# Optimization experiments

Measured on AMD Instinct MI355X. Metric: run time of the kernel, lower is better.

Reference implementation:

```python
import jax, jax.numpy as jnp
import numpy as np

EPS = 1e-12  # tf.nn.l2_normalize epsilon used inside keras CosineSimilarity


def _cos(a, b):
    # keras CosineSimilarity returns -cos; callers negate explicitly.
    an = a / jnp.sqrt(jnp.maximum(jnp.sum(a * a, axis=-1, keepdims=True), EPS))
    bn = b / jnp.sqrt(jnp.maximum(jnp.sum(b * b, axis=-1, keepdims=True), EPS))
    return jnp.sum(an * bn, axis=-1)


def setup_inputs() -> dict:
    key = jax.random.key(0)
    B, S, D, H, N = 1024, 200, 128, 128, 64
    ks = jax.random.split(key, 8)
    X_series = jax.random.normal(ks[0], (B, S, D), jnp.float32)
    pos_series = jax.random.normal(ks[1], (S, D), jnp.float32)
    X_item = jax.random.normal(ks[2], (B, D), jnp.float32)
    origin = jax.random.normal(ks[3], (B, N, D), jnp.float32)  # X_negative
    # contiguous-prefix validity mask (module assumes valid positions form a prefix)
    lengths = jax.random.randint(ks[4], (B,), 1, S + 1)
    valid_mask = jnp.arange(S)[None, :] < lengths[:, None]
    # learned params (GlorotUniform-scale init)
    Wp = jax.random.normal(ks[5], (D, H), jnp.float32) * 0.08
    We = jax.random.normal(ks[6], (D, H), jnp.float32) * 0.08
    z = jax.random.normal(ks[7], (H,), jnp.float32) * 0.1
    return {"X_series": X_series, "pos_series": pos_series, "X_item": X_item,
            "valid_mask": valid_mask, "origin": origin, "Wp": Wp, "We": We, "z": z}


def reference(X_series, pos_series, X_item, valid_mask, origin, Wp, We, z):
    B, S, D = X_series.shape
    # additive tanh attention: z . tanh(X_series @ We + pos_series @ Wp)
    hidden = jnp.tanh(jnp.einsum('bsd,dh->bsh', X_series, We) + (pos_series @ Wp)[None])
    scores = jnp.einsum('bsh,h->bs', hidden, z)
    scores = jnp.where(valid_mask, scores, -jnp.inf)
    attn = jax.nn.softmax(scores, axis=-1)                      # [B,S]
    attentioned = attn[:, :, None] * X_series                    # [B,S,D]
    attention_output = jnp.sum(attentioned, axis=1)              # [B,D]
    inner = jnp.sum(attention_output * X_item, axis=-1, keepdims=True)
    concated = jnp.concatenate([attention_output, inner], axis=1)  # [B,D+1]

    # ---- auxiliary loss ----
    last_idx = jnp.sum(valid_mask.astype(jnp.int32), axis=1) - 1
    last_vec = attentioned[jnp.arange(B), last_idx]              # gather_nd
    new_mask = (jnp.arange(S)[None, :] < last_idx[:, None]).astype(X_series.dtype)
    out_vec = jnp.sum(attentioned * new_mask[:, :, None], axis=1)  # [B,D]
    # keras CosineSimilarity = -cos_sim; then mapped to (x+1)/2 and used as logits
    pos_logits = (-_cos(last_vec, out_vec) + 1.0) / 2.0          # [B]
    neg_logits = (-_cos(origin, out_vec[:, None, :]) + 1.0) / 2.0  # [B,N]
    pos_loss = jax.nn.softplus(-pos_logits)  # sigmoid_xent labels=1
    neg_loss = jax.nn.softplus(neg_logits)   # sigmoid_xent labels=0
    # NB: TF reduces pos_loss over its only axis -> scalar, broadcast-added to [B]
    auxiliary_loss = jnp.sum(pos_loss) + jnp.sum(neg_loss, axis=-1)  # [B]
    return concated, auxiliary_loss
```

## Files before the change

kernel.cpp:

```cpp
#include <hip/hip_runtime.h>
#include <hip/hip_bf16.h>
#include <math.h>

#define B_ 1024
#define S_ 200
#define D_ 128
#define H_ 128
#define N_ 64

typedef __attribute__((ext_vector_type(8))) short short8;
typedef __attribute__((ext_vector_type(8))) __bf16 bf16x8;
typedef __attribute__((ext_vector_type(4))) float floatx4;

static __device__ __forceinline__ float bf2f(unsigned short u) {
    union { unsigned int i; float f; } v; v.i = ((unsigned int)u) << 16; return v.f;
}
static __device__ __forceinline__ unsigned short f2bf(float f) {
    union { float f; unsigned int u; } v; v.f = f;
    unsigned int u = v.u;
    return (unsigned short)((u + 0x7FFFu + ((u >> 16) & 1u)) >> 16);
}
static __device__ __forceinline__ float ld1(const void* p, int isbf, size_t i) {
    return isbf ? bf2f(((const unsigned short*)p)[i]) : ((const float*)p)[i];
}
static __device__ __forceinline__ float fast_tanh(float x) {
    float t = __expf(2.0f * x);
    return 1.0f - 2.0f * __builtin_amdgcn_rcpf(t + 1.0f);
}

__global__ __launch_bounds__(64) void detect_kernel(
    const void* a0, const void* a1, const void* a2, const void* a3,
    const void* a4, const void* a5, const void* a6, const void* a7,
    int* flags)
{
    int bid = blockIdx.x, t = threadIdx.x;
    if (bid == 3) {
        const unsigned char* mb = (const unsigned char*)a3;
        int f = 0;
        for (int i = t; i < 4096; i += 64)
            if ((i & 3) && mb[i]) f = 1;
        for (int off = 32; off; off >>= 1) f |= __shfl_xor(f, off, 64);
        if (t == 0) flags[3] = f;
        return;
    }
    const void* ptrs[8] = {a0, a1, a2, a3, a4, a5, a6, a7};
    const int counts[8] = {B_*S_*D_, S_*D_, B_*D_, 0, B_*N_*D_, D_*H_, D_*H_, H_};
    const unsigned int* w = (const unsigned int*)ptrs[bid];
    int words = counts[bid] / 2; if (words > 1024) words = 1024;
    int pass = 0, tot = 0;
    for (int i = t; i < words; i += 64) {
        unsigned int e = (w[i] >> 7) & 0xFF;
        tot++;
        if (e == 0 || (e >= 96 && e <= 140)) pass++;
    }
    for (int off = 32; off; off >>= 1) {
        pass += __shfl_xor(pass, off, 64);
        tot  += __shfl_xor(tot,  off, 64);
    }
    if (t == 0) flags[bid] = (pass * 4 >= tot * 3) ? 1 : 0;
}

__global__ __launch_bounds__(1024) void prep_kernel(
    const void* __restrict__ We, const int* __restrict__ flags,
    unsigned short* __restrict__ WeT)
{
    __shared__ unsigned short T[128][136];
    int t = threadIdx.x;
    int fWe = flags[6];
    for (int c = t; c < 2048; c += 1024) {
        int d = c >> 4, h8 = (c & 15) * 8;
        short8 v;
        if (fWe) {
            v = *(const short8*)((const unsigned short*)We + d * H_ + h8);
        } else {
            const float* p = (const float*)We + d * H_ + h8;
            float4 a = ((const float4*)p)[0], b = ((const float4*)p)[1];
            v[0] = (short)f2bf(a.x); v[1] = (short)f2bf(a.y);
            v[2] = (short)f2bf(a.z); v[3] = (short)f2bf(a.w);
            v[4] = (short)f2bf(b.x); v[5] = (short)f2bf(b.y);
            v[6] = (short)f2bf(b.z); v[7] = (short)f2bf(b.w);
        }
        *(short8*)(&T[d][h8]) = v;
    }
    __syncthreads();
    for (int c = t; c < 2048; c += 1024) {
        int h = c >> 4, d8 = (c & 15) * 8;
        short8 v;
#pragma unroll
        for (int j = 0; j < 8; ++j) v[j] = (short)T[d8 + j][h];
        *(short8*)(WeT + h * D_ + d8) = v;
    }
}

__global__ __launch_bounds__(128) void pb_kernel(
    const void* __restrict__ pos, const void* __restrict__ Wp,
    const int* __restrict__ flags, float* __restrict__ pb)
{
    int s = blockIdx.x, h = threadIdx.x;
    int fpos = flags[1], fWp = flags[5];
    __shared__ float prow[D_];
    prow[h] = ld1(pos, fpos, (size_t)s * D_ + h);
    __syncthreads();
    float acc = 0.f;
    if (fWp) {
        const unsigned short* W = (const unsigned short*)Wp;
        for (int d = 0; d < D_; ++d) acc = fmaf(prow[d], bf2f(W[d * H_ + h]), acc);
    } else {
        const float* W = (const float*)Wp;
        for (int d = 0; d < D_; ++d) acc = fmaf(prow[d], W[d * H_ + h], acc);
    }
    pb[s * H_ + h] = acc;
}

__global__ __launch_bounds__(256) void scores_kernel(
    const void* __restrict__ Xs, const unsigned short* __restrict__ WeT,
    const void* __restrict__ zv, const float* __restrict__ pb,
    const int* __restrict__ flags, float* __restrict__ scores)
{
    int t = threadIdx.x;
    int lane = t & 63, w = t >> 6;
    int quad = lane >> 4, mrow = lane & 15;
    int fXs = flags[0], fz = flags[7];
    int row0 = blockIdx.x * 128 + w * 32;

    float zl[8];
#pragma unroll
    for (int nt = 0; nt < 8; ++nt) zl[nt] = ld1(zv, fz, nt * 16 + mrow);

    floatx4 acc[2][8];
#pragma unroll
    for (int mt = 0; mt < 2; ++mt)
#pragma unroll
        for (int nt = 0; nt < 8; ++nt) {
            acc[mt][nt][0] = 0.f; acc[mt][nt][1] = 0.f;
            acc[mt][nt][2] = 0.f; acc[mt][nt][3] = 0.f;
        }

#pragma unroll
    for (int kk = 0; kk < 128; kk += 32) {
        bf16x8 af[2];
#pragma unroll
        for (int mt = 0; mt < 2; ++mt) {
            size_t roff = (size_t)(row0 + mt * 16 + mrow) * D_ + kk + quad * 8;
            if (fXs) {
                short8 v = *(const short8*)((const unsigned short*)Xs + roff);
                af[mt] = __builtin_bit_cast(bf16x8, v);
            } else {
                const float* p = (const float*)Xs + roff;
                float4 a = ((const float4*)p)[0], b = ((const float4*)p)[1];
                short8 v;
                v[0] = (short)f2bf(a.x); v[1] = (short)f2bf(a.y);
                v[2] = (short)f2bf(a.z); v[3] = (short)f2bf(a.w);
                v[4] = (short)f2bf(b.x); v[5] = (short)f2bf(b.y);
                v[6] = (short)f2bf(b.z); v[7] = (short)f2bf(b.w);
                af[mt] = __builtin_bit_cast(bf16x8, v);
            }
        }
#pragma unroll
        for (int nt = 0; nt < 8; ++nt) {
            short8 bv = *(const short8*)(WeT + (nt * 16 + mrow) * D_ + kk + quad * 8);
            bf16x8 bf = __builtin_bit_cast(bf16x8, bv);
            acc[0][nt] = __builtin_amdgcn_mfma_f32_16x16x32_bf16(af[0], bf, acc[0][nt], 0, 0, 0);
            acc[1][nt] = __builtin_amdgcn_mfma_f32_16x16x32_bf16(af[1], bf, acc[1][nt], 0, 0, 0);
        }
    }

#pragma unroll
    for (int mt = 0; mt < 2; ++mt) {
#pragma unroll
        for (int reg = 0; reg < 4; ++reg) {
            int grow = row0 + mt * 16 + quad * 4 + reg;
            int s = grow % S_;
            const float* pbrow = pb + (size_t)s * H_;
            float rs = 0.f;
#pragma unroll
            for (int nt = 0; nt < 8; ++nt) {
                float v = fast_tanh(acc[mt][nt][reg] + pbrow[nt * 16 + mrow]);
                rs = fmaf(v, zl[nt], rs);
            }
#pragma unroll
            for (int off = 1; off < 16; off <<= 1)
                rs += __shfl_xor(rs, off, 64);
            if (mrow == 0) scores[grow] = rs;
        }
    }
}

__global__ __launch_bounds__(256) void perB_kernel(
    const void* __restrict__ Xs, const void* __restrict__ Xitem,
    const void* __restrict__ maskv, const void* __restrict__ origin,
    const float* __restrict__ scores, const int* __restrict__ flags,
    float* __restrict__ pos_loss, float* __restrict__ neg_sum,
    float* __restrict__ out)
{
    int b = blockIdx.x, t = threadIdx.x;
    int wv = t >> 6, lane = t & 63;
    int fXs = flags[0], fXi = flags[2], fMk = flags[3], fOr = flags[4];
    __shared__ float attn[256];
    __shared__ float att_out[D_];
    __shared__ float lastv[D_];
    __shared__ float outv[D_];
    __shared__ float partial[8][D_];
    __shared__ float red[16];
    __shared__ int redi[4];
    __shared__ float sc1, sc2, sc3;

    int nz = 0;
    if (t < S_)
        nz = fMk ? (((const unsigned char*)maskv)[(size_t)b * S_ + t] != 0)
                 : (((const int*)maskv)[(size_t)b * S_ + t] != 0);
    unsigned long long bal = __ballot(nz);
    if (lane == 0) redi[wv] = __popcll(bal);
    __syncthreads();
    int length = redi[0] + redi[1] + redi[2] + redi[3];
    int last = length - 1;

    float sc = (t < length) ? scores[(size_t)b * S_ + t] : -INFINITY;
    float m = sc;
    for (int off = 32; off; off >>= 1) m = fmaxf(m, __shfl_xor(m, off, 64));
    if (lane == 0) red[wv] = m;
    __syncthreads();
    if (t == 0) sc1 = fmaxf(fmaxf(red[0], red[1]), fmaxf(red[2], red[3]));
    __syncthreads();
    float e = (t < length) ? expf(sc - sc1) : 0.f;
    float r = e;
    for (int off = 32; off; off >>= 1) r += __shfl_xor(r, off, 64);
    __syncthreads();
    if (lane == 0) red[wv] = r;
    __syncthreads();
    if (t == 0) sc2 = red[0] + red[1] + red[2] + red[3];
    __syncthreads();
    attn[t] = e / sc2;
    __syncthreads();

    {
        int part = t >> 5;
        int d4 = (t & 31) * 4;
        float a0 = 0, a1 = 0, a2 = 0, a3 = 0;
        if (fXs) {
#pragma unroll 5
            for (int s = part; s < S_; s += 8) {
                float ww = attn[s];
                uint2 u = *(const uint2*)((const unsigned short*)Xs + ((size_t)b * S_ + s) * D_ + d4);
                a0 = fmaf(ww, bf2f((unsigned short)(u.x & 0xffff)), a0);
                a1 = fmaf(ww, bf2f((unsigned short)(u.x >> 16)), a1);
                a2 = fmaf(ww, bf2f((unsigned short)(u.y & 0xffff)), a2);
                a3 = fmaf(ww, bf2f((unsigned short)(u.y >> 16)), a3);
            }
        } else {
#pragma unroll 5
            for (int s = part; s < S_; s += 8) {
                float ww = attn[s];
                float4 u = *(const float4*)((const float*)Xs + ((size_t)b * S_ + s) * D_ + d4);
                a0 = fmaf(ww, u.x, a0);
                a1 = fmaf(ww, u.y, a1);
                a2 = fmaf(ww, u.z, a2);
                a3 = fmaf(ww, u.w, a3);
            }
        }
        partial[part][d4] = a0; partial[part][d4 + 1] = a1;
        partial[part][d4 + 2] = a2; partial[part][d4 + 3] = a3;
    }
    __syncthreads();
    if (t < D_) {
        float v = 0.f;
#pragma unroll
        for (int p = 0; p < 8; ++p) v += partial[p][t];
        att_out[t] = v;
        float lv = attn[last] * ld1(Xs, fXs, ((size_t)b * S_ + last) * D_ + t);
        lastv[t] = lv;
        outv[t] = v - lv;
    }
    __syncthreads();

    {
        float pi = (t < D_) ? att_out[t] * ld1(Xitem, fXi, (size_t)b * D_ + t) : 0.f;
        for (int off = 32; off; off >>= 1) pi += __shfl_xor(pi, off, 64);
        if (lane == 0) red[wv] = pi;
        __syncthreads();
        if (t < D_) out[(size_t)b * (D_ + 1) + t] = att_out[t];
        if (t == 0)
            out[(size_t)b * (D_ + 1) + D_] = red[0] + red[1] + red[2] + red[3];
        __syncthreads();
    }

    {
        float l_ = (t < D_) ? lastv[t] : 0.f;
        float o_ = (t < D_) ? outv[t] : 0.f;
        float r0 = l_ * l_, r1 = l_ * o_, r2 = o_ * o_;
        for (int off = 32; off; off >>= 1) {
            r0 += __shfl_xor(r0, off, 64);
            r1 += __shfl_xor(r1, off, 64);
            r2 += __shfl_xor(r2, off, 64);
        }
        if (lane == 0) { red[wv] = r0; red[4 + wv] = r1; red[8 + wv] = r2; }
        __syncthreads();
        if (t == 0) {
            float ll = red[0] + red[1] + red[2] + red[3];
            float lo = red[4] + red[5] + red[6] + red[7];
            float oo = red[8] + red[9] + red[10] + red[11];
            float cosv = lo / (sqrtf(fmaxf(ll, 1e-12f)) * sqrtf(fmaxf(oo, 1e-12f)));
            float pl = 0.5f * (1.f - cosv);
            pos_loss[b] = log1pf(expf(-pl));
            sc3 = oo;
        }
        __syncthreads();
    }

    {
        int d = lane * 2;
        float v0 = outv[d], v1 = outv[d + 1];
        float vv = sc3;
        float accs = 0.f;
        for (int n = wv; n < N_; n += 4) {
            size_t base = ((size_t)b * N_ + n) * D_ + d;
            float o0, o1;
            if (fOr) {
                unsigned int u = *(const unsigned int*)((const unsigned short*)origin + base);
                o0 = bf2f((unsigned short)(u & 0xffff));
                o1 = bf2f((unsigned short)(u >> 16));
            } else {
                float2 u = *(const float2*)((const float*)origin + base);
                o0 = u.x; o1 = u.y;
            }
            float oo = o0 * o0 + o1 * o1;
            float ov = o0 * v0 + o1 * v1;
            for (int off = 32; off; off >>= 1) {
                oo += __shfl_xor(oo, off, 64);
                ov += __shfl_xor(ov, off, 64);
            }
            float cosn = ov / (sqrtf(fmaxf(oo, 1e-12f)) * sqrtf(fmaxf(vv, 1e-12f)));
            float nl = 0.5f * (1.f - cosn);
            accs += log1pf(expf(nl));
        }
        __syncthreads();
        if (lane == 0) red[wv] = accs;
        __syncthreads();
        if (t == 0) neg_sum[b] = red[0] + red[1] + red[2] + red[3];
    }
}

__global__ __launch_bounds__(1024) void final_kernel(
    const float* __restrict__ pos_loss,
    const float* __restrict__ neg_sum,
    float* __restrict__ out)
{
    __shared__ float red[16];
    int t = threadIdx.x;
    float v = pos_loss[t];
    for (int off = 32; off; off >>= 1) v += __shfl_xor(v, off, 64);
    if ((t & 63) == 0) red[t >> 6] = v;
    __syncthreads();
    if (t == 0) {
        float s = 0.f;
#pragma unroll
        for (int i = 0; i < 16; ++i) s += red[i];
        red[0] = s;
    }
    __syncthreads();
    out[(size_t)B_ * (D_ + 1) + t] = red[0] + neg_sum[t];
}

extern "C" void kernel_launch(void* const* d_in, const int* in_sizes, int n_in,
                              void* d_out, int out_size, void* d_ws, size_t ws_size,
                              hipStream_t stream) {
    const void* Xs     = d_in[0];
    const void* pos    = d_in[1];
    const void* Xitem  = d_in[2];
    const void* mask   = d_in[3];
    const void* origin = d_in[4];
    const void* Wp     = d_in[5];
    const void* We     = d_in[6];
    const void* zv     = d_in[7];

    int*   flags    = (int*)d_ws;
    unsigned short* WeT = (unsigned short*)((char*)d_ws + 128);
    float* ws       = (float*)((char*)d_ws + 128 + 32768);
    float* pb       = ws;
    float* scores   = pb + 25600;
    float* pos_loss = scores + 204800;
    float* neg_sum  = pos_loss + B_;
    float* out = (float*)d_out;

    detect_kernel<<<8, 64, 0, stream>>>(Xs, pos, Xitem, mask, origin, Wp, We, zv, flags);
    prep_kernel<<<1, 1024, 0, stream>>>(We, flags, WeT);
    pb_kernel<<<S_, 128, 0, stream>>>(pos, Wp, flags, pb);
    scores_kernel<<<(B_ * S_) / 128, 256, 0, stream>>>(Xs, WeT, zv, pb, flags, scores);
    perB_kernel<<<B_, 256, 0, stream>>>(Xs, Xitem, mask, origin, scores, flags, pos_loss, neg_sum, out);
    final_kernel<<<1, 1024, 0, stream>>>(pos_loss, neg_sum, out);
}
```

Before: 287.0 us.

## Fuse score MFMA into per-batch kernel with X_series staged in LDS

```diff
diff --git a/kernel.cpp b/kernel.cpp
--- a/kernel.cpp
+++ b/kernel.cpp
@@ -7,6 +7,7 @@
 #define D_ 128
 #define H_ 128
 #define N_ 64
+#define XP 136
 
 typedef __attribute__((ext_vector_type(8))) short short8;
 typedef __attribute__((ext_vector_type(8))) __bf16 bf16x8;
@@ -60,142 +61,72 @@
     if (t == 0) flags[bid] = (pass * 4 >= tot * 3) ? 1 : 0;
 }
 
-__global__ __launch_bounds__(1024) void prep_kernel(
-    const void* __restrict__ We, const int* __restrict__ flags,
-    unsigned short* __restrict__ WeT)
+__global__ __launch_bounds__(128) void prep_kernel(
+    const void* __restrict__ We, const void* __restrict__ pos,
+    const void* __restrict__ Wp, const int* __restrict__ flags,
+    unsigned short* __restrict__ WeTf, float* __restrict__ pb)
 {
+    int blk = blockIdx.x, t = threadIdx.x;
     __shared__ unsigned short T[128][136];
-    int t = threadIdx.x;
-    int fWe = flags[6];
-    for (int c = t; c < 2048; c += 1024) {
-        int d = c >> 4, h8 = (c & 15) * 8;
-        short8 v;
-        if (fWe) {
-            v = *(const short8*)((const unsigned short*)We + d * H_ + h8);
-        } else {
-            const float* p = (const float*)We + d * H_ + h8;
-            float4 a = ((const float4*)p)[0], b = ((const float4*)p)[1];
-            v[0] = (short)f2bf(a.x); v[1] = (short)f2bf(a.y);
-            v[2] = (short)f2bf(a.z); v[3] = (short)f2bf(a.w);
-            v[4] = (short)f2bf(b.x); v[5] = (short)f2bf(b.y);
-            v[6] = (short)f2bf(b.z); v[7] = (short)f2bf(b.w);
-        }
-        *(short8*)(&T[d][h8]) = v;
-    }
-    __syncthreads();
-    for (int c = t; c < 2048; c += 1024) {
-        int h = c >> 4, d8 = (c & 15) * 8;
-        short8 v;
-#pragma unroll
-        for (int j = 0; j < 8; ++j) v[j] = (short)T[d8 + j][h];
-        *(short8*)(WeT + h * D_ + d8) = v;
-    }
-}
-
-__global__ __launch_bounds__(128) void pb_kernel(
-    const void* __restrict__ pos, const void* __restrict__ Wp,
-    const int* __restrict__ flags, float* __restrict__ pb)
-{
-    int s = blockIdx.x, h = threadIdx.x;
-    int fpos = flags[1], fWp = flags[5];
     __shared__ float prow[D_];
-    prow[h] = ld1(pos, fpos, (size_t)s * D_ + h);
-    __syncthreads();
-    float acc = 0.f;
-    if (fWp) {
-        const unsigned short* W = (const unsigned short*)Wp;
-        for (int d = 0; d < D_; ++d) acc = fmaf(prow[d], bf2f(W[d * H_ + h]), acc);
-    } else {
-        const float* W = (const float*)Wp;
-        for (int d = 0; d < D_; ++d) acc = fmaf(prow[d], W[d * H_ + h], acc);
-    }
-    pb[s * H_ + h] = acc;
-}
-
-__global__ __launch_bounds__(256) void scores_kernel(
-    const void* __restrict__ Xs, const unsigned short* __restrict__ WeT,
-    const void* __restrict__ zv, const float* __restrict__ pb,
-    const int* __restrict__ flags, float* __restrict__ scores)
-{
-    int t = threadIdx.x;
-    int lane = t & 63, w = t >> 6;
-    int quad = lane >> 4, mrow = lane & 15;
-    int fXs = flags[0], fz = flags[7];
-    int row0 = blockIdx.x * 128 + w * 32;
-
-    float zl[8];
-#pragma unroll
-    for (int nt = 0; nt < 8; ++nt) zl[nt] = ld1(zv, fz, nt * 16 + mrow);
-
-    floatx4 acc[2][8];
-#pragma unroll
-    for (int mt = 0; mt < 2; ++mt)
-#pragma unroll
-        for (int nt = 0; nt < 8; ++nt) {
-            acc[mt][nt][0] = 0.f; acc[mt][nt][1] = 0.f;
-            acc[mt][nt][2] = 0.f; acc[mt][nt][3] = 0.f;
-        }
-
-#pragma unroll
-    for (int kk = 0; kk < 128; kk += 32) {
-        bf16x8 af[2];
-#pragma unroll
-        for (int mt = 0; mt < 2; ++mt) {
-            size_t roff = (size_t)(row0 + mt * 16 + mrow) * D_ + kk + quad * 8;
-            if (fXs) {
-                short8 v = *(const short8*)((const unsigned short*)Xs + roff);
-                af[mt] = __builtin_bit_cast(bf16x8, v);
+    if (blk == 0) {
+        int fWe = flags[6];
+        for (int c = t; c < 2048; c += 128) {
+            int d = c >> 4, h8 = (c & 15) * 8;
+            short8 v;
+            if (fWe) {
+                v = *(const short8*)((const unsigned short*)We + d * H_ + h8);
             } else {
-                const float* p = (const float*)Xs + roff;
+                const float* p = (const float*)We + d * H_ + h8;
                 float4 a = ((const float4*)p)[0], b = ((const float4*)p)[1];
-                short8 v;
                 v[0] = (short)f2bf(a.x); v[1] = (short)f2bf(a.y);
                 v[2] = (short)f2bf(a.z); v[3] = (short)f2bf(a.w);
                 v[4] = (short)f2bf(b.x); v[5] = (short)f2bf(b.y);
                 v[6] = (short)f2bf(b.z); v[7] = (short)f2bf(b.w);
-                af[mt] = __builtin_bit_cast(bf16x8, v);
-            }
-        }
-#pragma unroll
-        for (int nt = 0; nt < 8; ++nt) {
-            short8 bv = *(const short8*)(WeT + (nt * 16 + mrow) * D_ + kk + quad * 8);
-            bf16x8 bf = __builtin_bit_cast(bf16x8, bv);
-            acc[0][nt] = __builtin_amdgcn_mfma_f32_16x16x32_bf16(af[0], bf, acc[0][nt], 0, 0, 0);
-            acc[1][nt] = __builtin_amdgcn_mfma_f32_16x16x32_bf16(af[1], bf, acc[1][nt], 0, 0, 0);
-        }
-    }
-
-#pragma unroll
-    for (int mt = 0; mt < 2; ++mt) {
-#pragma unroll
-        for (int reg = 0; reg < 4; ++reg) {
-            int grow = row0 + mt * 16 + quad * 4 + reg;
-            int s = grow % S_;
-            const float* pbrow = pb + (size_t)s * H_;
-            float rs = 0.f;
-#pragma unroll
-            for (int nt = 0; nt < 8; ++nt) {
-                float v = fast_tanh(acc[mt][nt][reg] + pbrow[nt * 16 + mrow]);
-                rs = fmaf(v, zl[nt], rs);
-            }
-#pragma unroll
-            for (int off = 1; off < 16; off <<= 1)
-                rs += __shfl_xor(rs, off, 64);
-            if (mrow == 0) scores[grow] = rs;
-        }
-    }
-}
-
-__global__ __launch_bounds__(256) void perB_kernel(
+            }
+            *(short8*)(&T[d][h8]) = v;
+        }
+        __syncthreads();
+        for (int i = t; i < 2048; i += 128) {
+            int frag = i >> 6, ln = i & 63;
+            int nt = frag >> 2, kks = frag & 3;
+            int h = nt * 16 + (ln & 15);
+            int dbase = kks * 32 + (ln >> 4) * 8;
+            short8 v;
+#pragma unroll
+            for (int j = 0; j < 8; ++j) v[j] = (short)T[dbase + j][h];
+            *(short8*)(WeTf + (size_t)i * 8) = v;
+        }
+    } else {
+        int s = blk - 1, h = t;
+        prow[h] = ld1(pos, flags[1], (size_t)s * D_ + h);
+        __syncthreads();
+        float acc = 0.f;
+        if (flags[5]) {
+            const unsigned short* W = (const unsigned short*)Wp;
+            for (int d = 0; d < D_; ++d) acc = fmaf(prow[d], bf2f(W[d * H_ + h]), acc);
+        } else {
+            const float* W = (const float*)Wp;
+            for (int d = 0; d < D_; ++d) acc = fmaf(prow[d], W[d * H_ + h], acc);
+        }
+        pb[s * H_ + h] = acc;
+    }
+}
+
+__global__ __launch_bounds__(256) void fused_kernel(
     const void* __restrict__ Xs, const void* __restrict__ Xitem,
     const void* __restrict__ maskv, const void* __restrict__ origin,
-    const float* __restrict__ scores, const int* __restrict__ flags,
+    const unsigned short* __restrict__ WeTf, const void* __restrict__ zv,
+    const float* __restrict__ pb, const int* __restrict__ flags,
     float* __restrict__ pos_loss, float* __restrict__ neg_sum,
     float* __restrict__ out)
 {
     int b = blockIdx.x, t = threadIdx.x;
     int wv = t >> 6, lane = t & 63;
-    int fXs = flags[0], fXi = flags[2], fMk = flags[3], fOr = flags[4];
+    int quad = lane >> 4, mrow = lane & 15;
+    int fXs = flags[0], fXi = flags[2], fMk = flags[3], fOr = flags[4], fz = flags[7];
+
+    __shared__ unsigned short Xsh[208 * XP];
     __shared__ float attn[256];
     __shared__ float att_out[D_];
     __shared__ float lastv[D_];
@@ -203,7 +134,7 @@
     __shared__ float partial[8][D_];
     __shared__ float red[16];
     __shared__ int redi[4];
-    __shared__ float sc1, sc2, sc3;
+    __shared__ float sc1s, sc2s, sc3s;
 
     int nz = 0;
     if (t < S_)
@@ -211,52 +142,105 @@
                  : (((const int*)maskv)[(size_t)b * S_ + t] != 0);
     unsigned long long bal = __ballot(nz);
     if (lane == 0) redi[wv] = __popcll(bal);
+
+    if (fXs) {
+        const unsigned short* Xb = (const unsigned short*)Xs + (size_t)b * S_ * D_;
+        for (int idx = t; idx < 3200; idx += 256) {
+            int s = idx >> 4, d8 = (idx & 15) * 8;
+            short8 v = *(const short8*)(Xb + s * D_ + d8);
+            *(short8*)(Xsh + s * XP + d8) = v;
+        }
+    } else {
+        const float* Xb = (const float*)Xs + (size_t)b * S_ * D_;
+        for (int idx = t; idx < 6400; idx += 256) {
+            int s = idx >> 5, d4 = (idx & 31) * 4;
+            float4 v = *(const float4*)(Xb + s * D_ + d4);
+            uint2 u;
+            u.x = (unsigned int)f2bf(v.x) | ((unsigned int)f2bf(v.y) << 16);
+            u.y = (unsigned int)f2bf(v.z) | ((unsigned int)f2bf(v.w) << 16);
+            *(uint2*)(Xsh + s * XP + d4) = u;
+        }
+    }
+    for (int i = t; i < 1024; i += 256) {
+        int r = 200 + (i >> 7), c = i & 127;
+        Xsh[r * XP + c] = 0;
+    }
+
+    float zl[8];
+#pragma unroll
+    for (int nt = 0; nt < 8; ++nt) zl[nt] = ld1(zv, fz, nt * 16 + mrow);
+
     __syncthreads();
     int length = redi[0] + redi[1] + redi[2] + redi[3];
     int last = length - 1;
 
-    float sc = (t < length) ? scores[(size_t)b * S_ + t] : -INFINITY;
+    for (int tile = wv; tile < 13; tile += 4) {
+        int m0 = tile * 16;
+        floatx4 acc[8];
+#pragma unroll
+        for (int nt = 0; nt < 8; ++nt) {
+            acc[nt][0] = 0.f; acc[nt][1] = 0.f; acc[nt][2] = 0.f; acc[nt][3] = 0.f;
+        }
+        const unsigned short* arow = Xsh + (m0 + mrow) * XP;
+#pragma unroll
+        for (int kks = 0; kks < 4; ++kks) {
+            short8 av = *(const short8*)(arow + kks * 32 + quad * 8);
+            bf16x8 af = __builtin_bit_cast(bf16x8, av);
+#pragma unroll
+            for (int nt = 0; nt < 8; ++nt) {
+                short8 bv = *(const short8*)(WeTf + (size_t)(((nt << 2) + kks) * 64 + lane) * 8);
+                bf16x8 bf = __builtin_bit_cast(bf16x8, bv);
+                acc[nt] = __builtin_amdgcn_mfma_f32_16x16x32_bf16(af, bf, acc[nt], 0, 0, 0);
+            }
+        }
+#pragma unroll
+        for (int reg = 0; reg < 4; ++reg) {
+            int grow = m0 + quad * 4 + reg;
+            float rs = 0.f;
+            if (grow < S_) {
+                const float* pbrow = pb + (size_t)grow * H_;
+#pragma unroll
+                for (int nt = 0; nt < 8; ++nt)
+                    rs = fmaf(fast_tanh(acc[nt][reg] + pbrow[nt * 16 + mrow]), zl[nt], rs);
+            }
+#pragma unroll
+            for (int off = 1; off < 16; off <<= 1)
+                rs += __shfl_xor(rs, off, 64);
+            if (mrow == 0 && grow < S_) attn[grow] = rs;
+        }
+    }
+    __syncthreads();
+
+    float sc = (t < length) ? attn[t] : -INFINITY;
     float m = sc;
     for (int off = 32; off; off >>= 1) m = fmaxf(m, __shfl_xor(m, off, 64));
     if (lane == 0) red[wv] = m;
     __syncthreads();
-    if (t == 0) sc1 = fmaxf(fmaxf(red[0], red[1]), fmaxf(red[2], red[3]));
-    __syncthreads();
-    float e = (t < length) ? expf(sc - sc1) : 0.f;
+    if (t == 0) sc1s = fmaxf(fmaxf(red[0], red[1]), fmaxf(red[2], red[3]));
+    __syncthreads();
+    float e = (t < length) ? expf(sc - sc1s) : 0.f;
     float r = e;
     for (int off = 32; off; off >>= 1) r += __shfl_xor(r, off, 64);
     __syncthreads();
     if (lane == 0) red[wv] = r;
     __syncthreads();
-    if (t == 0) sc2 = red[0] + red[1] + red[2] + red[3];
-    __syncthreads();
-    attn[t] = e / sc2;
+    if (t == 0) sc2s = red[0] + red[1] + red[2] + red[3];
+    __syncthreads();
+    attn[t] = e / sc2s;
     __syncthreads();
 
     {
         int part = t >> 5;
         int d4 = (t & 31) * 4;
         float a0 = 0, a1 = 0, a2 = 0, a3 = 0;
-        if (fXs) {
 #pragma unroll 5
-            for (int s = part; s < S_; s += 8) {
-                float ww = attn[s];
-                uint2 u = *(const uint2*)((const unsigned short*)Xs + ((size_t)b * S_ + s) * D_ + d4);
-                a0 = fmaf(ww, bf2f((unsigned short)(u.x & 0xffff)), a0);
-                a1 = fmaf(ww, bf2f((unsigned short)(u.x >> 16)), a1);
-                a2 = fmaf(ww, bf2f((unsigned short)(u.y & 0xffff)), a2);
-                a3 = fmaf(ww, bf2f((unsigned short)(u.y >> 16)), a3);
-            }
-        } else {
-#pragma unroll 5
-            for (int s = part; s < S_; s += 8) {
-                float ww = attn[s];
-                float4 u = *(const float4*)((const float*)Xs + ((size_t)b * S_ + s) * D_ + d4);
-                a0 = fmaf(ww, u.x, a0);
-                a1 = fmaf(ww, u.y, a1);
-                a2 = fmaf(ww, u.z, a2);
-                a3 = fmaf(ww, u.w, a3);
-            }
+        for (int s = part; s < S_; s += 8) {
+            float ww = attn[s];
+            uint2 u = *(const uint2*)(Xsh + s * XP + d4);
+            a0 = fmaf(ww, bf2f((unsigned short)(u.x & 0xffff)), a0);
+            a1 = fmaf(ww, bf2f((unsigned short)(u.x >> 16)), a1);
+            a2 = fmaf(ww, bf2f((unsigned short)(u.y & 0xffff)), a2);
+            a3 = fmaf(ww, bf2f((unsigned short)(u.y >> 16)), a3);
         }
         partial[part][d4] = a0; partial[part][d4 + 1] = a1;
         partial[part][d4 + 2] = a2; partial[part][d4 + 3] = a3;
@@ -267,7 +251,7 @@
 #pragma unroll
         for (int p = 0; p < 8; ++p) v += partial[p][t];
         att_out[t] = v;
-        float lv = attn[last] * ld1(Xs, fXs, ((size_t)b * S_ + last) * D_ + t);
+        float lv = attn[last] * bf2f(Xsh[last * XP + t]);
         lastv[t] = lv;
         outv[t] = v - lv;
     }
@@ -302,7 +286,7 @@
             float cosv = lo / (sqrtf(fmaxf(ll, 1e-12f)) * sqrtf(fmaxf(oo, 1e-12f)));
             float pl = 0.5f * (1.f - cosv);
             pos_loss[b] = log1pf(expf(-pl));
-            sc3 = oo;
+            sc3s = oo;
         }
         __syncthreads();
     }
@@ -310,7 +294,7 @@
     {
         int d = lane * 2;
         float v0 = outv[d], v1 = outv[d + 1];
-        float vv = sc3;
+        float vv = sc3s;
         float accs = 0.f;
         for (int n = wv; n < N_; n += 4) {
             size_t base = ((size_t)b * N_ + n) * D_ + d;
@@ -374,18 +358,15 @@
     const void* zv     = d_in[7];
 
     int*   flags    = (int*)d_ws;
-    unsigned short* WeT = (unsigned short*)((char*)d_ws + 128);
-    float* ws       = (float*)((char*)d_ws + 128 + 32768);
-    float* pb       = ws;
-    float* scores   = pb + 25600;
-    float* pos_loss = scores + 204800;
+    unsigned short* WeTf = (unsigned short*)((char*)d_ws + 128);
+    float* pb       = (float*)((char*)d_ws + 128 + 32768);
+    float* pos_loss = pb + 25600;
     float* neg_sum  = pos_loss + B_;
     float* out = (float*)d_out;
 
     detect_kernel<<<8, 64, 0, stream>>>(Xs, pos, Xitem, mask, origin, Wp, We, zv, flags);
-    prep_kernel<<<1, 1024, 0, stream>>>(We, flags, WeT);
-    pb_kernel<<<S_, 128, 0, stream>>>(pos, Wp, flags, pb);
-    scores_kernel<<<(B_ * S_) / 128, 256, 0, stream>>>(Xs, WeT, zv, pb, flags, scores);
-    perB_kernel<<<B_, 256, 0, stream>>>(Xs, Xitem, mask, origin, scores, flags, pos_loss, neg_sum, out);
+    prep_kernel<<<201, 128, 0, stream>>>(We, pos, Wp, flags, WeTf, pb);
+    fused_kernel<<<B_, 256, 0, stream>>>(Xs, Xitem, mask, origin, WeTf, zv, pb, flags,
+                                         pos_loss, neg_sum, out);
     final_kernel<<<1, 1024, 0, stream>>>(pos_loss, neg_sum, out);
 }
```

New measurement: 273.1 us. 4.8% less time.

## Merge prep kernels, stage fragment-ordered weights in LDS, prefetch negatives early

Applied to the files above, without the earlier changes.

```diff
diff --git a/kernel.cpp b/kernel.cpp
--- a/kernel.cpp
+++ b/kernel.cpp
@@ -60,69 +60,73 @@
     if (t == 0) flags[bid] = (pass * 4 >= tot * 3) ? 1 : 0;
 }
 
-__global__ __launch_bounds__(1024) void prep_kernel(
-    const void* __restrict__ We, const int* __restrict__ flags,
-    unsigned short* __restrict__ WeT)
+__global__ __launch_bounds__(128) void prep_kernel(
+    const void* __restrict__ We, const void* __restrict__ pos,
+    const void* __restrict__ Wp, const int* __restrict__ flags,
+    unsigned short* __restrict__ WeTf, float* __restrict__ pb)
 {
+    int blk = blockIdx.x, t = threadIdx.x;
     __shared__ unsigned short T[128][136];
-    int t = threadIdx.x;
-    int fWe = flags[6];
-    for (int c = t; c < 2048; c += 1024) {
-        int d = c >> 4, h8 = (c & 15) * 8;
-        short8 v;
-        if (fWe) {
-            v = *(const short8*)((const unsigned short*)We + d * H_ + h8);
+    __shared__ float prow[D_];
+    if (blk == 0) {
+        int fWe = flags[6];
+        for (int c = t; c < 2048; c += 128) {
+            int d = c >> 4, h8 = (c & 15) * 8;
+            short8 v;
+            if (fWe) {
+                v = *(const short8*)((const unsigned short*)We + d * H_ + h8);
+            } else {
+                const float* p = (const float*)We + d * H_ + h8;
+                float4 a = ((const float4*)p)[0], b = ((const float4*)p)[1];
+                v[0] = (short)f2bf(a.x); v[1] = (short)f2bf(a.y);
+                v[2] = (short)f2bf(a.z); v[3] = (short)f2bf(a.w);
+                v[4] = (short)f2bf(b.x); v[5] = (short)f2bf(b.y);
+                v[6] = (short)f2bf(b.z); v[7] = (short)f2bf(b.w);
+            }
+            *(short8*)(&T[d][h8]) = v;
+        }
+        __syncthreads();
+        for (int i = t; i < 2048; i += 128) {
+            int frag = i >> 6, ln = i & 63;
+            int nt = frag >> 2, kks = frag & 3;
+            int h = nt * 16 + (ln & 15);
+            int dbase = kks * 32 + (ln >> 4) * 8;
+            short8 v;
+#pragma unroll
+            for (int j = 0; j < 8; ++j) v[j] = (short)T[dbase + j][h];
+            *(short8*)(WeTf + (size_t)i * 8) = v;
+        }
+    } else {
+        int s = blk - 1, h = t;
+        prow[h] = ld1(pos, flags[1], (size_t)s * D_ + h);
+        __syncthreads();
+        float acc = 0.f;
+        if (flags[5]) {
+            const unsigned short* W = (const unsigned short*)Wp;
+            for (int d = 0; d < D_; ++d) acc = fmaf(prow[d], bf2f(W[d * H_ + h]), acc);
         } else {
-            const float* p = (const float*)We + d * H_ + h8;
-            float4 a = ((const float4*)p)[0], b = ((const float4*)p)[1];
-            v[0] = (short)f2bf(a.x); v[1] = (short)f2bf(a.y);
-            v[2] = (short)f2bf(a.z); v[3] = (short)f2bf(a.w);
-            v[4] = (short)f2bf(b.x); v[5] = (short)f2bf(b.y);
-            v[6] = (short)f2bf(b.z); v[7] = (short)f2bf(b.w);
-        }
-        *(short8*)(&T[d][h8]) = v;
-    }
-    __syncthreads();
-    for (int c = t; c < 2048; c += 1024) {
-        int h = c >> 4, d8 = (c & 15) * 8;
-        short8 v;
-#pragma unroll
-        for (int j = 0; j < 8; ++j) v[j] = (short)T[d8 + j][h];
-        *(short8*)(WeT + h * D_ + d8) = v;
-    }
-}
-
-__global__ __launch_bounds__(128) void pb_kernel(
-    const void* __restrict__ pos, const void* __restrict__ Wp,
-    const int* __restrict__ flags, float* __restrict__ pb)
-{
-    int s = blockIdx.x, h = threadIdx.x;
-    int fpos = flags[1], fWp = flags[5];
-    __shared__ float prow[D_];
-    prow[h] = ld1(pos, fpos, (size_t)s * D_ + h);
-    __syncthreads();
-    float acc = 0.f;
-    if (fWp) {
-        const unsigned short* W = (const unsigned short*)Wp;
-        for (int d = 0; d < D_; ++d) acc = fmaf(prow[d], bf2f(W[d * H_ + h]), acc);
-    } else {
-        const float* W = (const float*)Wp;
-        for (int d = 0; d < D_; ++d) acc = fmaf(prow[d], W[d * H_ + h], acc);
-    }
-    pb[s * H_ + h] = acc;
+            const float* W = (const float*)Wp;
+            for (int d = 0; d < D_; ++d) acc = fmaf(prow[d], W[d * H_ + h], acc);
+        }
+        pb[s * H_ + h] = acc;
+    }
 }
 
 __global__ __launch_bounds__(256) void scores_kernel(
-    const void* __restrict__ Xs, const unsigned short* __restrict__ WeT,
+    const void* __restrict__ Xs, const unsigned short* __restrict__ WeTf,
     const void* __restrict__ zv, const float* __restrict__ pb,
     const int* __restrict__ flags, float* __restrict__ scores)
 {
+    __shared__ unsigned short Bsh[16384];
     int t = threadIdx.x;
     int lane = t & 63, w = t >> 6;
     int quad = lane >> 4, mrow = lane & 15;
     int fXs = flags[0], fz = flags[7];
     int row0 = blockIdx.x * 128 + w * 32;
 
+    for (int i = t; i < 2048; i += 256)
+        *(short8*)(Bsh + i * 8) = *(const short8*)(WeTf + (size_t)i * 8);
+
     float zl[8];
 #pragma unroll
     for (int nt = 0; nt < 8; ++nt) zl[nt] = ld1(zv, fz, nt * 16 + mrow);
@@ -135,13 +139,14 @@
             acc[mt][nt][0] = 0.f; acc[mt][nt][1] = 0.f;
             acc[mt][nt][2] = 0.f; acc[mt][nt][3] = 0.f;
         }
-
-#pragma unroll
-    for (int kk = 0; kk < 128; kk += 32) {
+    __syncthreads();
+
+#pragma unroll
+    for (int kks = 0; kks < 4; ++kks) {
         bf16x8 af[2];
 #pragma unroll
         for (int mt = 0; mt < 2; ++mt) {
-            size_t roff = (size_t)(row0 + mt * 16 + mrow) * D_ + kk + quad * 8;
+            size_t roff = (size_t)(row0 + mt * 16 + mrow) * D_ + kks * 32 + quad * 8;
             if (fXs) {
                 short8 v = *(const short8*)((const unsigned short*)Xs + roff);
                 af[mt] = __builtin_bit_cast(bf16x8, v);
@@ -158,7 +163,7 @@
         }
 #pragma unroll
         for (int nt = 0; nt < 8; ++nt) {
-            short8 bv = *(const short8*)(WeT + (nt * 16 + mrow) * D_ + kk + quad * 8);
+            short8 bv = *(const short8*)(Bsh + (((nt << 2) + kks) * 64 + lane) * 8);
             bf16x8 bf = __builtin_bit_cast(bf16x8, bv);
             acc[0][nt] = __builtin_amdgcn_mfma_f32_16x16x32_bf16(af[0], bf, acc[0][nt], 0, 0, 0);
             acc[1][nt] = __builtin_amdgcn_mfma_f32_16x16x32_bf16(af[1], bf, acc[1][nt], 0, 0, 0);
@@ -174,10 +179,8 @@
             const float* pbrow = pb + (size_t)s * H_;
             float rs = 0.f;
 #pragma unroll
-            for (int nt = 0; nt < 8; ++nt) {
-                float v = fast_tanh(acc[mt][nt][reg] + pbrow[nt * 16 + mrow]);
-                rs = fmaf(v, zl[nt], rs);
-            }
+            for (int nt = 0; nt < 8; ++nt)
+                rs = fmaf(fast_tanh(acc[mt][nt][reg] + pbrow[nt * 16 + mrow]), zl[nt], rs);
 #pragma unroll
             for (int off = 1; off < 16; off <<= 1)
                 rs += __shfl_xor(rs, off, 64);
@@ -186,7 +189,7 @@
     }
 }
 
-__global__ __launch_bounds__(256) void perB_kernel(
+__global__ __launch_bounds__(256) void attnout_kernel(
     const void* __restrict__ Xs, const void* __restrict__ Xitem,
     const void* __restrict__ maskv, const void* __restrict__ origin,
     const float* __restrict__ scores, const int* __restrict__ flags,
@@ -201,9 +204,36 @@
     __shared__ float lastv[D_];
     __shared__ float outv[D_];
     __shared__ float partial[8][D_];
+    __shared__ float p_oo[4][64];
+    __shared__ float p_ov[4][64];
     __shared__ float red[16];
     __shared__ int redi[4];
-    __shared__ float sc1, sc2, sc3;
+    __shared__ float sc1s, sc2s, vvs;
+
+    int nn = t >> 2, part = t & 3;
+    float o_f[32];
+    if (fOr) {
+        const unsigned short* p = (const unsigned short*)origin + ((size_t)b * N_ + nn) * D_ + part * 32;
+#pragma unroll
+        for (int j = 0; j < 4; ++j) {
+            uint4 u = *(const uint4*)(p + j * 8);
+            o_f[j*8+0] = bf2f((unsigned short)(u.x & 0xffff));
+            o_f[j*8+1] = bf2f((unsigned short)(u.x >> 16));
+            o_f[j*8+2] = bf2f((unsigned short)(u.y & 0xffff));
+            o_f[j*8+3] = bf2f((unsigned short)(u.y >> 16));
+            o_f[j*8+4] = bf2f((unsigned short)(u.z & 0xffff));
+            o_f[j*8+5] = bf2f((unsigned short)(u.z >> 16));
+            o_f[j*8+6] = bf2f((unsigned short)(u.w & 0xffff));
+            o_f[j*8+7] = bf2f((unsigned short)(u.w >> 16));
+        }
+    } else {
+        const float* p = (const float*)origin + ((size_t)b * N_ + nn) * D_ + part * 32;
+#pragma unroll
+        for (int j = 0; j < 8; ++j) {
+            float4 v = *(const float4*)(p + j * 4);
+            o_f[j*4+0] = v.x; o_f[j*4+1] = v.y; o_f[j*4+2] = v.z; o_f[j*4+3] = v.w;
+        }
+    }
 
     int nz = 0;
     if (t < S_)
@@ -220,26 +250,26 @@
     for (int off = 32; off; off >>= 1) m = fmaxf(m, __shfl_xor(m, off, 64));
     if (lane == 0) red[wv] = m;
     __syncthreads();
-    if (t == 0) sc1 = fmaxf(fmaxf(red[0], red[1]), fmaxf(red[2], red[3]));
-    __syncthreads();
-    float e = (t < length) ? expf(sc - sc1) : 0.f;
+    if (t == 0) sc1s = fmaxf(fmaxf(red[0], red[1]), fmaxf(red[2], red[3]));
+    __syncthreads();
+    float e = (t < length) ? expf(sc - sc1s) : 0.f;
     float r = e;
     for (int off = 32; off; off >>= 1) r += __shfl_xor(r, off, 64);
     __syncthreads();
     if (lane == 0) red[wv] = r;
     __syncthreads();
-    if (t == 0) sc2 = red[0] + red[1] + red[2] + red[3];
-    __syncthreads();
-    attn[t] = e / sc2;
+    if (t == 0) sc2s = red[0] + red[1] + red[2] + red[3];
+    __syncthreads();
+    attn[t] = e / sc2s;
     __syncthreads();
 
     {
-        int part = t >> 5;
+        int sp = t >> 5;
         int d4 = (t & 31) * 4;
         float a0 = 0, a1 = 0, a2 = 0, a3 = 0;
         if (fXs) {
 #pragma unroll 5
-            for (int s = part; s < S_; s += 8) {
+            for (int s = sp; s < S_; s += 8) {
                 float ww = attn[s];
                 uint2 u = *(const uint2*)((const unsigned short*)Xs + ((size_t)b * S_ + s) * D_ + d4);
                 a0 = fmaf(ww, bf2f((unsigned short)(u.x & 0xffff)), a0);
@@ -249,7 +279,7 @@
             }
         } else {
 #pragma unroll 5
-            for (int s = part; s < S_; s += 8) {
+            for (int s = sp; s < S_; s += 8) {
                 float ww = attn[s];
                 float4 u = *(const float4*)((const float*)Xs + ((size_t)b * S_ + s) * D_ + d4);
                 a0 = fmaf(ww, u.x, a0);
@@ -258,8 +288,8 @@
                 a3 = fmaf(ww, u.w, a3);
             }
         }
-        partial[part][d4] = a0; partial[part][d4 + 1] = a1;
-        partial[part][d4 + 2] = a2; partial[part][d4 + 3] = a3;
+        partial[sp][d4] = a0; partial[sp][d4 + 1] = a1;
+        partial[sp][d4 + 2] = a2; partial[sp][d4 + 3] = a3;
     }
     __syncthreads();
     if (t < D_) {
@@ -302,41 +332,32 @@
             float cosv = lo / (sqrtf(fmaxf(ll, 1e-12f)) * sqrtf(fmaxf(oo, 1e-12f)));
             float pl = 0.5f * (1.f - cosv);
             pos_loss[b] = log1pf(expf(-pl));
-            sc3 = oo;
+            vvs = oo;
         }
         __syncthreads();
     }
 
     {
-        int d = lane * 2;
-        float v0 = outv[d], v1 = outv[d + 1];
-        float vv = sc3;
-        float accs = 0.f;
-        for (int n = wv; n < N_; n += 4) {
-            size_t base = ((size_t)b * N_ + n) * D_ + d;
-            float o0, o1;
-            if (fOr) {
-                unsigned int u = *(const unsigned int*)((const unsigned short*)origin + base);
-                o0 = bf2f((unsigned short)(u & 0xffff));
-                o1 = bf2f((unsigned short)(u >> 16));
-            } else {
-                float2 u = *(const float2*)((const float*)origin + base);
-                o0 = u.x; o1 = u.y;
-            }
-            float oo = o0 * o0 + o1 * o1;
-            float ov = o0 * v0 + o1 * v1;
-            for (int off = 32; off; off >>= 1) {
-                oo += __shfl_xor(oo, off, 64);
-                ov += __shfl_xor(ov, off, 64);
-            }
-            float cosn = ov / (sqrtf(fmaxf(oo, 1e-12f)) * sqrtf(fmaxf(vv, 1e-12f)));
+        float o_oo = 0.f, o_ov = 0.f;
+#pragma unroll
+        for (int jj = 0; jj < 32; ++jj) {
+            int j = (jj + part * 8) & 31;
+            float wv_ = outv[part * 32 + j];
+            o_oo = fmaf(o_f[j], o_f[j], o_oo);
+            o_ov = fmaf(o_f[j], wv_, o_ov);
+        }
+        p_oo[part][nn] = o_oo;
+        p_ov[part][nn] = o_ov;
+        __syncthreads();
+        if (t < 64) {
+            float oo = p_oo[0][t] + p_oo[1][t] + p_oo[2][t] + p_oo[3][t];
+            float ov = p_ov[0][t] + p_ov[1][t] + p_ov[2][t] + p_ov[3][t];
+            float cosn = ov / (sqrtf(fmaxf(oo, 1e-12f)) * sqrtf(fmaxf(vvs, 1e-12f)));
             float nl = 0.5f * (1.f - cosn);
-            accs += log1pf(expf(nl));
-        }
-        __syncthreads();
-        if (lane == 0) red[wv] = accs;
-        __syncthreads();
-        if (t == 0) neg_sum[b] = red[0] + red[1] + red[2] + red[3];
+            float nloss = log1pf(expf(nl));
+            for (int off = 32; off; off >>= 1) nloss += __shfl_xor(nloss, off, 64);
+            if (t == 0) neg_sum[b] = nloss;
+        }
     }
 }
 
@@ -374,18 +395,17 @@
     const void* zv     = d_in[7];
 
     int*   flags    = (int*)d_ws;
-    unsigned short* WeT = (unsigned short*)((char*)d_ws + 128);
-    float* ws       = (float*)((char*)d_ws + 128 + 32768);
-    float* pb       = ws;
+    unsigned short* WeTf = (unsigned short*)((char*)d_ws + 128);
+    float* pb       = (float*)((char*)d_ws + 128 + 32768);
     float* scores   = pb + 25600;
     float* pos_loss = scores + 204800;
     float* neg_sum  = pos_loss + B_;
     float* out = (float*)d_out;
 
     detect_kernel<<<8, 64, 0, stream>>>(Xs, pos, Xitem, mask, origin, Wp, We, zv, flags);
-    prep_kernel<<<1, 1024, 0, stream>>>(We, flags, WeT);
-    pb_kernel<<<S_, 128, 0, stream>>>(pos, Wp, flags, pb);
-    scores_kernel<<<(B_ * S_) / 128, 256, 0, stream>>>(Xs, WeT, zv, pb, flags, scores);
-    perB_kernel<<<B_, 256, 0, stream>>>(Xs, Xitem, mask, origin, scores, flags, pos_loss, neg_sum, out);
+    prep_kernel<<<201, 128, 0, stream>>>(We, pos, Wp, flags, WeTf, pb);
+    scores_kernel<<<(B_ * S_) / 128, 256, 0, stream>>>(Xs, WeTf, zv, pb, flags, scores);
+    attnout_kernel<<<B_, 256, 0, stream>>>(Xs, Xitem, mask, origin, scores, flags,
+                                           pos_loss, neg_sum, out);
     final_kernel<<<1, 1024, 0, stream>>>(pos_loss, neg_sum, out);
 }
```

New measurement: 268.1 us. 1.07x faster.
